# Kernel optimization log

Hardware: AMD Instinct MI355X
Metric: run time of the kernel (lower is better)

## Reference

```python
import jax, jax.numpy as jnp
import numpy as np

K = 3      # deformable kernel size
PAD = 1    # padding for all 3x3 convs


def conv2d(x, w, b):
    y = jax.lax.conv_general_dilated(x, w, (1, 1), ((PAD, PAD), (PAD, PAD)),
                                     dimension_numbers=('NCHW', 'OIHW', 'NCHW'))
    return y + b[None, :, None, None]


def ln_channels(x, w, b, eps=1e-5):
    # Restormer 'WithBias' LayerNorm: normalize over channel dim of NCHW
    mu = jnp.mean(x, axis=1, keepdims=True)
    var = jnp.mean((x - mu) ** 2, axis=1, keepdims=True)
    return (x - mu) / jnp.sqrt(var + eps) * w[None, :, None, None] + b[None, :, None, None]


def deform_conv(x, offset, mask, weight, bias):
    # x: [B,Cin,H,W], offset: [B,2*K*K,H,W] (dy,dx interleaved), mask: [B,K*K,H,W]
    B, Cin, H, W = x.shape
    Kk = K * K
    off = offset.reshape(B, Kk, 2, H, W)
    dy, dx = off[:, :, 0], off[:, :, 1]                     # [B,Kk,H,W]
    ky, kx = jnp.meshgrid(jnp.arange(K), jnp.arange(K), indexing='ij')
    ky = (ky.reshape(-1) - PAD).astype(x.dtype)             # [Kk]
    kx = (kx.reshape(-1) - PAD).astype(x.dtype)
    py = jnp.arange(H, dtype=x.dtype)[None, None, :, None] + ky[None, :, None, None] + dy
    px = jnp.arange(W, dtype=x.dtype)[None, None, None, :] + kx[None, :, None, None] + dx
    y0 = jnp.floor(py); x0 = jnp.floor(px)
    wy1 = py - y0; wx1 = px - x0
    xf = x.reshape(B, Cin, H * W)

    def corner(yc, xc, wgt):
        valid = (yc >= 0) & (yc <= H - 1) & (xc >= 0) & (xc <= W - 1)
        yi = jnp.clip(yc, 0, H - 1).astype(jnp.int32)
        xi = jnp.clip(xc, 0, W - 1).astype(jnp.int32)
        idx = (yi * W + xi).reshape(B, -1)                  # [B, Kk*H*W]
        v = jax.vmap(lambda xb, ib: xb[:, ib])(xf, idx)     # [B, Cin, Kk*H*W]
        v = v.reshape(B, Cin, Kk, H, W)
        return v * (wgt * valid.astype(x.dtype))[:, None]

    sampled = (corner(y0, x0, (1 - wy1) * (1 - wx1))
               + corner(y0, x0 + 1, (1 - wy1) * wx1)
               + corner(y0 + 1, x0, wy1 * (1 - wx1))
               + corner(y0 + 1, x0 + 1, wy1 * wx1))         # [B,Cin,Kk,H,W]
    sampled = sampled * mask[:, None]                        # modulated (DCNv2)
    wk = weight.reshape(weight.shape[0], Cin, Kk)            # [Cout,Cin,Kk]
    out = jnp.einsum('bckhw,ock->bohw', sampled, wk)
    return out + bias[None, :, None, None]


def setup_inputs() -> dict:
    key = jax.random.key(0)
    ks = jax.random.split(key, 12)
    B, Ce, Cf, H, W = 4, 32, 64, 128, 128
    Cin, Kk = Ce + Cf, K * K
    d = {
        'f_evt_rec': jax.random.normal(ks[0], (B, Ce, H, W), jnp.float32),
        'f_efnet':   jax.random.normal(ks[1], (B, Cf, H, W), jnp.float32),
        'ln_evt_w': jnp.ones((Ce,), jnp.float32), 'ln_evt_b': jnp.zeros((Ce,), jnp.float32),
        'ln_ef_w':  jnp.ones((Cf,), jnp.float32), 'ln_ef_b':  jnp.zeros((Cf,), jnp.float32),
        'ln_al_w':  jnp.ones((Cf,), jnp.float32), 'ln_al_b':  jnp.zeros((Cf,), jnp.float32),
        'off_w': jax.random.normal(ks[2], (2 * Kk, Cin, K, K), jnp.float32) * 0.01,
        'off_b': jnp.zeros((2 * Kk,), jnp.float32),
        'mod_w': jax.random.normal(ks[3], (Kk, Cin, K, K), jnp.float32) * 0.01,
        'mod_b': jnp.zeros((Kk,), jnp.float32),
        'reg_w': jax.random.normal(ks[4], (Cf, Cin, K, K), jnp.float32) * 0.05,
        'reg_b': jnp.zeros((Cf,), jnp.float32),
        'stage_idx': 0,
    }
    return d


def reference(f_evt_rec, f_efnet, ln_evt_w, ln_evt_b, ln_ef_w, ln_ef_b,
              ln_al_w, ln_al_b, off_w, off_b, mod_w, mod_b, reg_w, reg_b, stage_idx):
    e = ln_channels(f_evt_rec, ln_evt_w, ln_evt_b)
    fe = ln_channels(f_efnet, ln_ef_w, ln_ef_b)
    ox = jnp.concatenate([e, fe], axis=1)                    # [B,96,H,W]
    offset = conv2d(ox, off_w, off_b)
    mask = 2.0 * jax.nn.sigmoid(conv2d(ox, mod_w, mod_b))
    al = deform_conv(ox, offset, mask, reg_w, reg_b)         # [B,64,H,W]
    al = jnp.where(al >= 0, al, 0.2 * al)                    # LeakyReLU(0.2)
    al = ln_channels(al, ln_al_w, ln_al_b)
    return al
```

## Files before the change

kernel.cpp:

```cpp
#include <hip/hip_runtime.h>
#include <hip/hip_bf16.h>

#define BATCH 4
#define HH 128
#define WW 128
#define CE 32
#define CF 64
#define CIN 96
#define COUT 64

typedef __bf16 bf16x8 __attribute__((ext_vector_type(8)));
typedef float f32x4 __attribute__((ext_vector_type(4)));
#define MFMA16(a, b, c) __builtin_amdgcn_mfma_f32_16x16x32_bf16(a, b, c, 0, 0, 0)
typedef union { uint4 u; bf16x8 v; } U8;

#define OX_BYTES   (BATCH * HH * WW * CIN * 2)
#define WCT_OFFB   OX_BYTES
#define WCT_BYTES  (27 * 32 * 32 * 2)
#define WKT_OFFB   (WCT_OFFB + WCT_BYTES)


__global__ __launch_bounds__(256) void ln_concat_prep(
    const float* __restrict__ evt, const float* __restrict__ efn,
    const float* __restrict__ w_e, const float* __restrict__ b_e,
    const float* __restrict__ w_f, const float* __restrict__ b_f,
    const float* __restrict__ off_w, const float* __restrict__ mod_w,
    const float* __restrict__ reg_w,
    __hip_bfloat16* __restrict__ ox,
    __hip_bfloat16* __restrict__ wcombT2,
    __hip_bfloat16* __restrict__ wkT2) {
  __shared__ float vals[64 * 97];
  __shared__ float part[4 * 64 * 4];
  __shared__ float stat[64 * 4];

  {
    int e = blockIdx.x * 256 + threadIdx.x;
    const int TOT1 = 27 * 32 * 32;
    const int TOT2 = 27 * 64 * 32;
    if (e < TOT1) {
      int r = e & 31, g = e >> 5;
      int oc = g & 31, tks = g >> 5;
      int tap = tks / 3, ks = tks % 3, c = ks * 32 + r;
      float v = 0.f;
      if (oc < 18)      v = off_w[(oc * CIN + c) * 9 + tap];
      else if (oc < 27) v = mod_w[((oc - 18) * CIN + c) * 9 + tap];
      wcombT2[e] = __float2bfloat16(v);
    } else if (e < TOT1 + TOT2) {
      int e2 = e - TOT1;
      int r = e2 & 31, g = e2 >> 5;
      int oc = g & 63, tks = g >> 6;
      int tap = tks / 3, ks = tks % 3, c = ks * 32 + r;
      wkT2[e2] = __float2bfloat16(reg_w[(oc * CIN + c) * 9 + tap]);
    }
  }

  int bid = blockIdx.x;
  int wg = (bid & 7) * 128 + (bid >> 3);
  int p0 = wg * 64;
  int b = p0 >> 14, y = (p0 >> 7) & 127, x0 = p0 & 127;
  int t = threadIdx.x, px = t & 63, g = t >> 6;

  float sE = 0.f, sE2 = 0.f, sF = 0.f, sF2 = 0.f;
  const float* pe = evt + (((size_t)b * CE) << 14) + (y << 7) + x0 + px;
#pragma unroll
  for (int j = 0; j < 8; ++j) {
    int c = g * 8 + j;
    float v = pe[(size_t)c << 14];
    vals[px * 97 + c] = v; sE += v; sE2 += v * v;
  }
  const float* pf = efn + (((size_t)b * CF) << 14) + (y << 7) + x0 + px;
#pragma unroll
  for (int j = 0; j < 16; ++j) {
    int c = g * 16 + j;
    float v = pf[(size_t)c << 14];
    vals[px * 97 + CE + c] = v; sF += v; sF2 += v * v;
  }
  {
    float4 p4 = {sE, sE2, sF, sF2};
    *(float4*)&part[(g * 64 + px) * 4] = p4;
  }
  __syncthreads();
  if (g == 0) {
    float aE = 0.f, aE2 = 0.f, aF = 0.f, aF2 = 0.f;
#pragma unroll
    for (int gg = 0; gg < 4; ++gg) {
      float4 p4 = *(const float4*)&part[(gg * 64 + px) * 4];
      aE += p4.x; aE2 += p4.y; aF += p4.z; aF2 += p4.w;
    }
    float muE = aE * (1.f / CE);
    float vE = aE2 * (1.f / CE) - muE * muE;
    float muF = aF * (1.f / CF);
    float vF = aF2 * (1.f / CF) - muF * muF;
    float4 s4 = {muE, rsqrtf(vE + 1e-5f), muF, rsqrtf(vF + 1e-5f)};
    *(float4*)&stat[px * 4] = s4;
  }
  __syncthreads();
  uint* orow = (uint*)(ox + (size_t)p0 * CIN);
#pragma unroll
  for (int i = 0; i < 12; ++i) {
    int e = i * 256 + t;
    int xx = e / 48, c = (e % 48) * 2;
    float v0 = vals[xx * 97 + c], v1 = vals[xx * 97 + c + 1];
    float mu, rs, lw0, lb0, lw1, lb1;
    if (c < CE) {
      mu = stat[xx * 4 + 0]; rs = stat[xx * 4 + 1];
      lw0 = w_e[c]; lb0 = b_e[c]; lw1 = w_e[c + 1]; lb1 = b_e[c + 1];
    } else {
      mu = stat[xx * 4 + 2]; rs = stat[xx * 4 + 3];
      lw0 = w_f[c - CE]; lb0 = b_f[c - CE]; lw1 = w_f[c + 1 - CE]; lb1 = b_f[c + 1 - CE];
    }
    float o0 = (v0 - mu) * rs * lw0 + lb0;
    float o1 = (v1 - mu) * rs * lw1 + lb1;
    __hip_bfloat16 h0 = __float2bfloat16(o0), h1 = __float2bfloat16(o1);
    orow[e] = ((uint)*(unsigned short*)&h1 << 16) | (uint)*(unsigned short*)&h0;
  }
}

__device__ __forceinline__ uint blend1(uint u0, uint u1, uint u2, uint u3,
                                       float w0, float w1, float w2, float w3) {
  float lo = w0 * __uint_as_float(u0 << 16) + w1 * __uint_as_float(u1 << 16)
           + w2 * __uint_as_float(u2 << 16) + w3 * __uint_as_float(u3 << 16);
  float hi = w0 * __uint_as_float(u0 & 0xffff0000u) + w1 * __uint_as_float(u1 & 0xffff0000u)
           + w2 * __uint_as_float(u2 & 0xffff0000u) + w3 * __uint_as_float(u3 & 0xffff0000u);
  __hip_bfloat16 bl = __float2bfloat16(lo), bh = __float2bfloat16(hi);
  return ((uint)*(unsigned short*)&bh << 16) | (uint)*(unsigned short*)&bl;
}

__global__ __launch_bounds__(256) void conv_deform_fused(
    const __hip_bfloat16* __restrict__ ox,
    const __hip_bfloat16* __restrict__ wct2,
    const __hip_bfloat16* __restrict__ wkt2,
    const float* __restrict__ off_b, const float* __restrict__ mod_b,
    const float* __restrict__ reg_b,
    const float* __restrict__ lnw, const float* __restrict__ lnb,
    float* __restrict__ out) {
  __shared__ short win[5 * 69 * CIN];
  __shared__ float offm[64 * 28];
  float* outl = (float*)win;

  int bid = blockIdx.x;
  int wg = (bid & 7) * 128 + (bid >> 3);
  int p0 = wg * 64;
  int b = p0 >> 14, y = (p0 >> 7) & 127, x0 = p0 & 127;
  const __hip_bfloat16* oxb = ox + (((size_t)b) << 14) * CIN;

  int t = threadIdx.x, lane = t & 63, wv = t >> 6;
  int lr = lane & 15, lg = lane >> 4;
  int pxw = (wv << 4) + lr;

  for (int u = t; u < 5 * 69 * 12; u += 256) {
    int c8 = u % 12, pos = u / 12;
    int wr = pos / 69, wc = pos % 69;
    int gy = y - 2 + wr, gx = x0 - 2 + wc;
    uint4 v = {0u, 0u, 0u, 0u};
    if ((unsigned)gy < 128u && (unsigned)gx < 128u)
      v = *(const uint4*)(oxb + (size_t)((gy << 7) + gx) * CIN + c8 * 8);
    *(uint4*)&win[pos * CIN + c8 * 8] = v;
  }
  __syncthreads();

  f32x4 cc0 = {0.f,0.f,0.f,0.f}, cc1 = {0.f,0.f,0.f,0.f};
#pragma unroll
  for (int tap = 0; tap < 9; ++tap) {
    int wr = tap / 3 + 1;
    int wc = pxw + tap % 3 + 1;
    const short* ar = &win[(wr * 69 + wc) * CIN + lg * 8];
#pragma unroll
    for (int ks = 0; ks < 3; ++ks) {
      bf16x8 a = *(const bf16x8*)(ar + ks * 32);
      const __hip_bfloat16* wb = wct2 + (size_t)((tap * 3 + ks) * 32) * 32 + lg * 8;
      U8 w0, w1;
      w0.u = *(const uint4*)(wb + lr * 32);
      w1.u = *(const uint4*)(wb + (16 + lr) * 32);
      cc0 = MFMA16(a, w0.v, cc0);
      cc1 = MFMA16(a, w1.v, cc1);
    }
  }
#pragma unroll
  for (int nt = 0; nt < 2; ++nt) {
    int oc = nt * 16 + lr;
    if (oc < 27) {
      float bia = (oc < 18) ? off_b[oc] : mod_b[oc - 18];
      f32x4 a = nt ? cc1 : cc0;
#pragma unroll
      for (int r = 0; r < 4; ++r) {
        float v = a[r] + bia;
        if (oc >= 18) v = 2.f / (1.f + __expf(-v));
        offm[((wv << 4) + (lg << 2) + r) * 28 + oc] = v;
      }
    }
  }

  const float* om = offm + pxw * 28;
  f32x4 ac0 = {0.f,0.f,0.f,0.f}, ac1 = {0.f,0.f,0.f,0.f};
  f32x4 ac2 = {0.f,0.f,0.f,0.f}, ac3 = {0.f,0.f,0.f,0.f};

#pragma unroll
  for (int tap = 0; tap < 9; ++tap) {
    float dyv = om[2 * tap], dxv = om[2 * tap + 1], mk = om[18 + tap];
    float psy = (float)(y + tap / 3 - 1) + dyv;
    float psx = (float)(x0 + pxw + tap % 3 - 1) + dxv;
    float fy = floorf(psy), fx = floorf(psx);
    float wy1 = psy - fy, wx1 = psx - fx;
    float wy0 = 1.f - wy1, wx0 = 1.f - wx1;
    int iy0 = (int)fy, ix0 = (int)fx, iy1 = iy0 + 1, ix1 = ix0 + 1;
    float vy0 = ((unsigned)iy0 < 128u) ? 1.f : 0.f;
    float vy1 = ((unsigned)iy1 < 128u) ? 1.f : 0.f;
    float vx0 = ((unsigned)ix0 < 128u) ? 1.f : 0.f;
    float vx1 = ((unsigned)ix1 < 128u) ? 1.f : 0.f;
    int cy0 = min(max(iy0, 0), 127), cy1 = min(max(iy1, 0), 127);
    int cx0 = min(max(ix0, 0), 127), cx1 = min(max(ix1, 0), 127);
    float pw0 = wy0 * wx0 * vy0 * vx0 * mk;
    float pw1 = wy0 * wx1 * vy0 * vx1 * mk;
    float pw2 = wy1 * wx0 * vy1 * vx0 * mk;
    float pw3 = wy1 * wx1 * vy1 * vx1 * mk;
    int ra = cy0 - y + 2, rb = cy1 - y + 2;
    int ca = cx0 - x0 + 2, cb = cx1 - x0 + 2;
    bool ina = (unsigned)ra < 5u, inb = (unsigned)rb < 5u;
    bool inca = (unsigned)ca < 69u, incb = (unsigned)cb < 69u;
    int w0o = (ina && inca) ? (ra * 69 + ca) * CIN : -1;
    int w1o = (ina && incb) ? (ra * 69 + cb) * CIN : -1;
    int w2o = (inb && inca) ? (rb * 69 + ca) * CIN : -1;
    int w3o = (inb && incb) ? (rb * 69 + cb) * CIN : -1;
    int g0 = ((cy0 << 7) + cx0) * CIN, g1 = ((cy0 << 7) + cx1) * CIN;
    int g2 = ((cy1 << 7) + cx0) * CIN, g3 = ((cy1 << 7) + cx1) * CIN;

#pragma unroll
    for (int ks = 0; ks < 3; ++ks) {
      int koff = ks * 32 + lg * 8;
      U8 q0, q1, q2, q3;
      q0.v = *(const bf16x8*)&win[(w0o < 0 ? 0 : w0o) + koff];
      q1.v = *(const bf16x8*)&win[(w1o < 0 ? 0 : w1o) + koff];
      q2.v = *(const bf16x8*)&win[(w2o < 0 ? 0 : w2o) + koff];
      q3.v = *(const bf16x8*)&win[(w3o < 0 ? 0 : w3o) + koff];
      if (w0o < 0) q0.u = *(const uint4*)(oxb + g0 + koff);
      if (w1o < 0) q1.u = *(const uint4*)(oxb + g1 + koff);
      if (w2o < 0) q2.u = *(const uint4*)(oxb + g2 + koff);
      if (w3o < 0) q3.u = *(const uint4*)(oxb + g3 + koff);
      U8 fa;
      fa.u.x = blend1(q0.u.x, q1.u.x, q2.u.x, q3.u.x, pw0, pw1, pw2, pw3);
      fa.u.y = blend1(q0.u.y, q1.u.y, q2.u.y, q3.u.y, pw0, pw1, pw2, pw3);
      fa.u.z = blend1(q0.u.z, q1.u.z, q2.u.z, q3.u.z, pw0, pw1, pw2, pw3);
      fa.u.w = blend1(q0.u.w, q1.u.w, q2.u.w, q3.u.w, pw0, pw1, pw2, pw3);
      const __hip_bfloat16* wb = wkt2 + (size_t)((tap * 3 + ks) * 64) * 32 + lg * 8;
      U8 b0, b1, b2, b3;
      b0.u = *(const uint4*)(wb + lr * 32);
      b1.u = *(const uint4*)(wb + (16 + lr) * 32);
      b2.u = *(const uint4*)(wb + (32 + lr) * 32);
      b3.u = *(const uint4*)(wb + (48 + lr) * 32);
      ac0 = MFMA16(fa.v, b0.v, ac0);
      ac1 = MFMA16(fa.v, b1.v, ac1);
      ac2 = MFMA16(fa.v, b2.v, ac2);
      ac3 = MFMA16(fa.v, b3.v, ac3);
    }
  }
  __syncthreads();

#pragma unroll
  for (int nt = 0; nt < 4; ++nt) {
    int oc = nt * 16 + lr;
    float bia = reg_b[oc];
    f32x4 a = (nt == 0) ? ac0 : (nt == 1) ? ac1 : (nt == 2) ? ac2 : ac3;
#pragma unroll
    for (int r = 0; r < 4; ++r) {
      float v = a[r] + bia;
      v = (v >= 0.f) ? v : 0.2f * v;
      outl[((wv << 4) + (lg << 2) + r) * 65 + oc] = v;
    }
  }
  {
    int px2 = (wv << 4) + (lane >> 2), part = lane & 3;
    float s = 0.f, s2 = 0.f;
#pragma unroll
    for (int j = 0; j < 16; ++j) {
      float v = outl[px2 * 65 + part * 16 + j];
      s += v; s2 += v * v;
    }
    s += __shfl_xor(s, 1); s2 += __shfl_xor(s2, 1);
    s += __shfl_xor(s, 2); s2 += __shfl_xor(s2, 2);
    float mu = s * (1.f / 64.f);
    float var = s2 * (1.f / 64.f) - mu * mu;
    float rs = rsqrtf(var + 1e-5f);
    size_t ob = (size_t)b * COUT * 16384 + (size_t)y * 128 + x0 + px2;
#pragma unroll
    for (int j = 0; j < 16; ++j) {
      int oc = part * 16 + j;
      float v = outl[px2 * 65 + oc];
      out[ob + (size_t)oc * 16384] = (v - mu) * rs * lnw[oc] + lnb[oc];
    }
  }
}

extern "C" void kernel_launch(void* const* d_in, const int* in_sizes, int n_in,
                              void* d_out, int out_size, void* d_ws, size_t ws_size,
                              hipStream_t stream) {
  const float* evt      = (const float*)d_in[0];
  const float* efn      = (const float*)d_in[1];
  const float* ln_evt_w = (const float*)d_in[2];
  const float* ln_evt_b = (const float*)d_in[3];
  const float* ln_ef_w  = (const float*)d_in[4];
  const float* ln_ef_b  = (const float*)d_in[5];
  const float* ln_al_w  = (const float*)d_in[6];
  const float* ln_al_b  = (const float*)d_in[7];
  const float* off_w    = (const float*)d_in[8];
  const float* off_b    = (const float*)d_in[9];
  const float* mod_w    = (const float*)d_in[10];
  const float* mod_b    = (const float*)d_in[11];
  const float* reg_w    = (const float*)d_in[12];
  const float* reg_b    = (const float*)d_in[13];
  float* out = (float*)d_out;

  char* wsb = (char*)d_ws;
  __hip_bfloat16* oxb    = (__hip_bfloat16*)wsb;
  __hip_bfloat16* wct2   = (__hip_bfloat16*)(wsb + WCT_OFFB);
  __hip_bfloat16* wkt2   = (__hip_bfloat16*)(wsb + WKT_OFFB);

  ln_concat_prep<<<BATCH * HH * WW / 64, 256, 0, stream>>>(
      evt, efn, ln_evt_w, ln_evt_b, ln_ef_w, ln_ef_b,
      off_w, mod_w, reg_w, oxb, wct2, wkt2);
  conv_deform_fused<<<BATCH * HH * WW / 64, 256, 0, stream>>>(
      oxb, wct2, wkt2, off_b, mod_b, reg_b, ln_al_w, ln_al_b, out);
}
```

Before: 167.4 us.

## Tile fused deform conv as 2x32 pixel blocks with padded LDS stride

Each workgroup now covers a 2-row by 32-column pixel tile instead of a 1x64 strip, so the staged input halo window shrinks from 5x69 to 6x36 positions. The LDS row stride is padded from 96 to 104 bf16 and the offset buffer stride from 28 to 29, to cut LDS bank conflicts. The squarer tile stages less halo per block and is meant to keep more of the deformable samples inside the shared window. Samples with large horizontal offsets now land outside the narrower window more often and fall back to global loads.

```diff
diff --git a/kernel.cpp b/kernel.cpp
--- a/kernel.cpp
+++ b/kernel.cpp
@@ -8,6 +8,11 @@
 #define CF 64
 #define CIN 96
 #define COUT 64
+
+#define WROWS 6
+#define WCOLS 36
+#define WSTR 104
+#define OFFSTR 29
 
 typedef __bf16 bf16x8 __attribute__((ext_vector_type(8)));
 typedef float f32x4 __attribute__((ext_vector_type(4)));
@@ -134,37 +139,40 @@
     const float* __restrict__ reg_b,
     const float* __restrict__ lnw, const float* __restrict__ lnb,
     float* __restrict__ out) {
-  __shared__ short win[5 * 69 * CIN];
-  __shared__ float offm[64 * 28];
+  __shared__ short win[WROWS * WCOLS * WSTR];
+  __shared__ float offm[64 * OFFSTR];
   float* outl = (float*)win;
 
   int bid = blockIdx.x;
   int wg = (bid & 7) * 128 + (bid >> 3);
-  int p0 = wg * 64;
-  int b = p0 >> 14, y = (p0 >> 7) & 127, x0 = p0 & 127;
+  int b = wg >> 8;
+  int rem = wg & 255;
+  int y0 = (rem >> 2) * 2;
+  int x0 = (rem & 3) * 32;
   const __hip_bfloat16* oxb = ox + (((size_t)b) << 14) * CIN;
 
   int t = threadIdx.x, lane = t & 63, wv = t >> 6;
   int lr = lane & 15, lg = lane >> 4;
-  int pxw = (wv << 4) + lr;
-
-  for (int u = t; u < 5 * 69 * 12; u += 256) {
+  int pxrow = wv >> 1;
+  int pxcol = ((wv & 1) << 4) + lr;
+
+  for (int u = t; u < WROWS * WCOLS * 12; u += 256) {
     int c8 = u % 12, pos = u / 12;
-    int wr = pos / 69, wc = pos % 69;
-    int gy = y - 2 + wr, gx = x0 - 2 + wc;
+    int wr = pos / WCOLS, wc = pos % WCOLS;
+    int gy = y0 - 2 + wr, gx = x0 - 2 + wc;
     uint4 v = {0u, 0u, 0u, 0u};
     if ((unsigned)gy < 128u && (unsigned)gx < 128u)
       v = *(const uint4*)(oxb + (size_t)((gy << 7) + gx) * CIN + c8 * 8);
-    *(uint4*)&win[pos * CIN + c8 * 8] = v;
+    *(uint4*)&win[pos * WSTR + c8 * 8] = v;
   }
   __syncthreads();
 
   f32x4 cc0 = {0.f,0.f,0.f,0.f}, cc1 = {0.f,0.f,0.f,0.f};
 #pragma unroll
   for (int tap = 0; tap < 9; ++tap) {
-    int wr = tap / 3 + 1;
-    int wc = pxw + tap % 3 + 1;
-    const short* ar = &win[(wr * 69 + wc) * CIN + lg * 8];
+    int wr = pxrow + tap / 3 + 1;
+    int wc = pxcol + tap % 3 + 1;
+    const short* ar = &win[(wr * WCOLS + wc) * WSTR + lg * 8];
 #pragma unroll
     for (int ks = 0; ks < 3; ++ks) {
       bf16x8 a = *(const bf16x8*)(ar + ks * 32);
@@ -186,20 +194,20 @@
       for (int r = 0; r < 4; ++r) {
         float v = a[r] + bia;
         if (oc >= 18) v = 2.f / (1.f + __expf(-v));
-        offm[((wv << 4) + (lg << 2) + r) * 28 + oc] = v;
+        offm[((wv << 4) + (lg << 2) + r) * OFFSTR + oc] = v;
       }
     }
   }
 
-  const float* om = offm + pxw * 28;
+  const float* om = offm + ((wv << 4) + lr) * OFFSTR;
   f32x4 ac0 = {0.f,0.f,0.f,0.f}, ac1 = {0.f,0.f,0.f,0.f};
   f32x4 ac2 = {0.f,0.f,0.f,0.f}, ac3 = {0.f,0.f,0.f,0.f};
 
 #pragma unroll
   for (int tap = 0; tap < 9; ++tap) {
     float dyv = om[2 * tap], dxv = om[2 * tap + 1], mk = om[18 + tap];
-    float psy = (float)(y + tap / 3 - 1) + dyv;
-    float psx = (float)(x0 + pxw + tap % 3 - 1) + dxv;
+    float psy = (float)(y0 + pxrow + tap / 3 - 1) + dyv;
+    float psx = (float)(x0 + pxcol + tap % 3 - 1) + dxv;
     float fy = floorf(psy), fx = floorf(psx);
     float wy1 = psy - fy, wx1 = psx - fx;
     float wy0 = 1.f - wy1, wx0 = 1.f - wx1;
@@ -214,14 +222,14 @@
     float pw1 = wy0 * wx1 * vy0 * vx1 * mk;
     float pw2 = wy1 * wx0 * vy1 * vx0 * mk;
     float pw3 = wy1 * wx1 * vy1 * vx1 * mk;
-    int ra = cy0 - y + 2, rb = cy1 - y + 2;
+    int ra = cy0 - y0 + 2, rb = cy1 - y0 + 2;
     int ca = cx0 - x0 + 2, cb = cx1 - x0 + 2;
-    bool ina = (unsigned)ra < 5u, inb = (unsigned)rb < 5u;
-    bool inca = (unsigned)ca < 69u, incb = (unsigned)cb < 69u;
-    int w0o = (ina && inca) ? (ra * 69 + ca) * CIN : -1;
-    int w1o = (ina && incb) ? (ra * 69 + cb) * CIN : -1;
-    int w2o = (inb && inca) ? (rb * 69 + ca) * CIN : -1;
-    int w3o = (inb && incb) ? (rb * 69 + cb) * CIN : -1;
+    bool ina = (unsigned)ra < (unsigned)WROWS, inb = (unsigned)rb < (unsigned)WROWS;
+    bool inca = (unsigned)ca < (unsigned)WCOLS, incb = (unsigned)cb < (unsigned)WCOLS;
+    int w0o = (ina && inca) ? (ra * WCOLS + ca) * WSTR : -1;
+    int w1o = (ina && incb) ? (ra * WCOLS + cb) * WSTR : -1;
+    int w2o = (inb && inca) ? (rb * WCOLS + ca) * WSTR : -1;
+    int w3o = (inb && incb) ? (rb * WCOLS + cb) * WSTR : -1;
     int g0 = ((cy0 << 7) + cx0) * CIN, g1 = ((cy0 << 7) + cx1) * CIN;
     int g2 = ((cy1 << 7) + cx0) * CIN, g3 = ((cy1 << 7) + cx1) * CIN;
 
@@ -270,6 +278,7 @@
   }
   {
     int px2 = (wv << 4) + (lane >> 2), part = lane & 3;
+    int orow = px2 >> 5, ocol = px2 & 31;
     float s = 0.f, s2 = 0.f;
 #pragma unroll
     for (int j = 0; j < 16; ++j) {
@@ -281,7 +290,7 @@
     float mu = s * (1.f / 64.f);
     float var = s2 * (1.f / 64.f) - mu * mu;
     float rs = rsqrtf(var + 1e-5f);
-    size_t ob = (size_t)b * COUT * 16384 + (size_t)y * 128 + x0 + px2;
+    size_t ob = (size_t)b * COUT * 16384 + (size_t)(y0 + orow) * 128 + x0 + ocol;
 #pragma unroll
     for (int j = 0; j < 16; ++j) {
       int oc = part * 16 + j;
```

After: 162.8 us. 2.8% less time.
